# Performance work log

Hardware: AMD Instinct MI355X
Metric: run time of the kernel (lower is better)

The kernel has to match this reference:

```python
import jax, jax.numpy as jnp
import numpy as np

D_STATE = 128   # Mamba2 default (the SS2D d_state=16 is never forwarded to Mamba2)
N_HEADS = 4     # d_ssm // headdim = d_model / (d_model//4)
D_CONV = 4
EPS = 1e-5


def silu(v):
    return v * jax.nn.sigmoid(v)


def setup_inputs() -> dict:
    key = jax.random.key(0)
    ks = jax.random.split(key, 12)
    d_model = 256
    d_inner = 2 * d_model            # expand=2
    d_ssm = d_model
    conv_dim = d_ssm + 2 * D_STATE   # 512
    d_in_proj = 2 * d_inner + 2 * D_STATE + N_HEADS  # 1284
    B, H, W = 8, 64, 64
    inp = {
        "x": jax.random.normal(ks[0], (B, d_model, H, W), jnp.float32),
        "in_proj_w": jax.random.normal(ks[1], (d_in_proj, d_model), jnp.float32) * 0.02,
        "conv_w": jax.random.normal(ks[2], (conv_dim, D_CONV), jnp.float32) * 0.2,
        "conv_b": jnp.zeros((conv_dim,), jnp.float32),
        "dt_bias": jax.random.normal(ks[3], (N_HEADS,), jnp.float32) * 0.1,
        "A_log": jnp.log(jax.random.uniform(ks[4], (N_HEADS,), jnp.float32, 1.0, 16.0)),
        "D": jax.random.normal(ks[5], (N_HEADS,), jnp.float32),
        "norm_w": jnp.ones((d_ssm,), jnp.float32),
        "out_proj_w": jax.random.normal(ks[6], (d_model, d_inner), jnp.float32) * 0.02,
        "se_w1": jax.random.normal(ks[7], (d_model // 4, d_model), jnp.float32) * 0.05,
        "se_b1": jnp.zeros((d_model // 4,), jnp.float32),
        "se_w2": jax.random.normal(ks[8], (d_model, d_model // 4), jnp.float32) * 0.05,
        "se_b2": jnp.zeros((d_model,), jnp.float32),
    }
    return inp


def _forward(x, in_proj_w, conv_w, conv_b, dt_bias, A_log, D, norm_w,
             out_proj_w, se_w1, se_b1, se_w2, se_b2):
    Bb, C, H, W = x.shape
    L = H * W
    d_model = C
    d_inner = 2 * d_model
    d_ssm = d_model
    d_mlp = d_inner - d_ssm
    headdim = d_ssm // N_HEADS
    conv_dim = d_ssm + 2 * D_STATE

    u = x.reshape(Bb, C, L).transpose(0, 2, 1)              # (b, l, c)
    zxbcdt = u @ in_proj_w.T                                 # (b, l, 1284)
    z0 = zxbcdt[..., :d_mlp]
    x0 = zxbcdt[..., d_mlp:2 * d_mlp]
    z = zxbcdt[..., 2 * d_mlp:2 * d_mlp + d_ssm]
    xBC = zxbcdt[..., 2 * d_mlp + d_ssm:2 * d_mlp + d_ssm + conv_dim]
    dt = zxbcdt[..., -N_HEADS:]

    dt = jax.nn.softplus(dt + dt_bias)                       # (b, l, h)

    # causal depthwise conv along l, kernel size D_CONV
    xpad = jnp.pad(xBC, ((0, 0), (D_CONV - 1, 0), (0, 0)))
    xconv = conv_b
    for k in range(D_CONV):
        xconv = xconv + xpad[:, k:k + L, :] * conv_w[:, k]
    xconv = silu(xconv)

    xs = xconv[..., :d_ssm]
    Bm = xconv[..., d_ssm:d_ssm + D_STATE]                   # (b, l, n) ngroups=1
    Cm = xconv[..., d_ssm + D_STATE:]                        # (b, l, n)
    xh = xs.reshape(Bb, L, N_HEADS, headdim)                 # (b, l, h, p)

    A = -jnp.exp(A_log)                                      # (h,)

    def step(hstate, inp):
        xt, dtt, Bt, Ct = inp  # (b,h,p), (b,h), (b,n), (b,n)
        dA = jnp.exp(dtt * A)                                # (b, h)
        hstate = hstate * dA[:, :, None, None] + \
            (dtt[:, :, None, None] * xt[..., None]) * Bt[:, None, None, :]
        y = jnp.einsum('bhpn,bn->bhp', hstate, Ct)
        return hstate, y

    h0 = jnp.zeros((Bb, N_HEADS, headdim, D_STATE), x.dtype)
    _, ys = jax.lax.scan(
        step, h0,
        (xh.transpose(1, 0, 2, 3), dt.transpose(1, 0, 2),
         Bm.transpose(1, 0, 2), Cm.transpose(1, 0, 2)))
    y = ys.transpose(1, 0, 2, 3)                             # (b, l, h, p)
    y = y + D[None, None, :, None] * xh                      # skip
    y = y.reshape(Bb, L, d_ssm)

    # gated RMSNorm (norm_before_gate=False): gate then normalize
    y = y * silu(z)
    y = y * jax.lax.rsqrt(jnp.mean(y * y, axis=-1, keepdims=True) + EPS) * norm_w

    y = jnp.concatenate([silu(z0) * x0, y], axis=-1)         # (b, l, d_inner)
    out = y @ out_proj_w.T                                   # (b, l, d_model)
    out = out.transpose(0, 2, 1).reshape(Bb, C, H, W)

    # SE-style spectral attention
    s = out.mean(axis=(2, 3))                                # (b, c)
    s = jax.nn.relu(s @ se_w1.T + se_b1)
    s = jax.nn.sigmoid(s @ se_w2.T + se_b2)
    return out * s[:, :, None, None]


def reference(x, in_proj_w, conv_w, conv_b, dt_bias, A_log, D, norm_w,
              out_proj_w, se_w1, se_b1, se_w2, se_b2):
    return _forward(x, in_proj_w, conv_w, conv_b, dt_bias, A_log, D, norm_w,
                    out_proj_w, se_w1, se_b1, se_w2, se_b2)
```

## Files before the change

### kernel.cpp

```cpp
#include <hip/hip_runtime.h>
#include <stdint.h>

typedef __attribute__((ext_vector_type(8))) short bf16x8;
typedef __attribute__((ext_vector_type(4))) float f32x4;

__device__ __forceinline__ float bf2f(unsigned short u) {
  unsigned int x = ((unsigned int)u) << 16;
  return __builtin_bit_cast(float, x);
}
__device__ __forceinline__ unsigned short f2bf(float f) {
  unsigned int x = __builtin_bit_cast(unsigned int, f);
  unsigned int r = x + 0x7FFFu + ((x >> 16) & 1u);
  return (unsigned short)(r >> 16);
}
__device__ __forceinline__ float silu(float v) { return v / (1.f + __expf(-v)); }
__device__ __forceinline__ f32x4 fz4() { f32x4 z; z[0]=0.f; z[1]=0.f; z[2]=0.f; z[3]=0.f; return z; }

#define LSEQ 4096
#define DMODEL 256
#define NIN 1284
#define NINP 1408

__global__ __launch_bounds__(256) void k_prep(const float* __restrict__ w_in,
                                              const float* __restrict__ w_out,
                                              unsigned short* __restrict__ wpad,
                                              unsigned short* __restrict__ woutbf,
                                              const float* __restrict__ x,
                                              unsigned short* __restrict__ ubf) {
  int bid = blockIdx.x;
  int tid = threadIdx.x;
  if (bid < 1920) {
    int idx = bid * 256 + tid;
    const int tot1 = NINP * DMODEL;
    if (idx < tot1) {
      int n = idx / DMODEL, k = idx % DMODEL;
      int src = (n < 512) ? ((n & 1) ? 256 + (n >> 1) : (n >> 1)) : n;
      float v = (src < NIN) ? w_in[src * DMODEL + k] : 0.f;
      wpad[idx] = f2bf(v);
    } else {
      int j = idx - tot1;
      woutbf[j] = f2bf(w_out[j]);
    }
    return;
  }
  __shared__ float t[64][65];
  int r = (bid - 1920) & 255;
  int b = (bid - 1920) >> 8;
  int lt = r >> 2, kt = r & 3;
  int l0 = lt * 64, k0 = kt * 64;
  int j = tid & 63, i0 = tid >> 6;
  for (int rr = 0; rr < 16; rr++) {
    int ki = i0 + rr * 4;
    t[ki][j] = x[(size_t)(b * DMODEL + k0 + ki) * LSEQ + l0 + j];
  }
  __syncthreads();
  for (int rr = 0; rr < 16; rr++) {
    int li = i0 + rr * 4;
    ubf[(size_t)(b * LSEQ + l0 + li) * DMODEL + k0 + j] = f2bf(t[j][li]);
  }
}

template <int KDIM, int LDA, int LDB, int EPI>
__global__ __launch_bounds__(256) void k_gemm(const unsigned short* __restrict__ A,
                                              const unsigned short* __restrict__ B,
                                              float* __restrict__ outF,
                                              unsigned short* __restrict__ outBF,
                                              unsigned short* __restrict__ outBF2,
                                              float* __restrict__ dtb, int tilesN) {
  __shared__ __align__(16) short lds[17408];
  short* As = lds;
  short* Bs = lds + 8192;
  int nwg = gridDim.x;
  int orig = blockIdx.x;
  int wgid = (nwg & 7) ? orig : ((orig & 7) * (nwg >> 3) + (orig >> 3));
  int tn = wgid % tilesN, tm = wgid / tilesN;
  int m0 = tm * 128, n0 = tn * 128;
  int tid = threadIdx.x;
  int w = tid >> 6, lane = tid & 63;
  int wr = w >> 1, wc = w & 1;
  f32x4 acc[4][4];
  for (int i = 0; i < 4; i++)
    for (int j = 0; j < 4; j++) acc[i][j] = fz4();

  for (int kt = 0; kt < KDIM / 64; kt++) {
    int k0 = kt * 64;
    for (int i = 0; i < 4; i++) {
      int rowblk = w * 32 + i * 8;
      int row = rowblk + (lane >> 3);
      int kc = ((lane & 7) ^ (row & 7)) * 8;
      const unsigned short* ga = A + (size_t)(m0 + row) * LDA + k0 + kc;
      __builtin_amdgcn_global_load_lds((const __attribute__((address_space(1))) unsigned int*)ga,
                                       (__attribute__((address_space(3))) unsigned int*)&As[rowblk * 64],
                                       16, 0, 0);
      const unsigned short* gb = B + (size_t)(n0 + row) * LDB + k0 + kc;
      __builtin_amdgcn_global_load_lds((const __attribute__((address_space(1))) unsigned int*)gb,
                                       (__attribute__((address_space(3))) unsigned int*)&Bs[rowblk * 64],
                                       16, 0, 0);
    }
    __syncthreads();
    for (int kk = 0; kk < 64; kk += 32) {
      int gq = (kk >> 3) + (lane >> 4);
      bf16x8 af[4], bfr[4];
      for (int mi = 0; mi < 4; mi++) {
        int rt = wr * 64 + mi * 16 + (lane & 15);
        af[mi] = *(const bf16x8*)((const char*)As + rt * 128 + ((gq ^ (rt & 7)) << 4));
      }
      for (int ni = 0; ni < 4; ni++) {
        int rs = wc * 64 + ni * 16 + (lane & 15);
        bfr[ni] = *(const bf16x8*)((const char*)Bs + rs * 128 + ((gq ^ (rs & 7)) << 4));
      }
      for (int mi = 0; mi < 4; mi++)
        for (int ni = 0; ni < 4; ni++)
          acc[mi][ni] = __builtin_amdgcn_mfma_f32_16x16x32_bf16(af[mi], bfr[ni], acc[mi][ni], 0, 0, 0);
    }
    __syncthreads();
  }

  int fq = lane >> 4, fr = lane & 15;
  if constexpr (EPI == 1) {
    short* Ct = lds;
    for (int mi = 0; mi < 4; mi++)
      for (int ni = 0; ni < 4; ni++)
        for (int j = 0; j < 4; j++) {
          int r = wr * 64 + mi * 16 + fq * 4 + j;
          int cch = wc * 64 + ni * 16 + fr;
          Ct[cch * 136 + r] = (short)f2bf(acc[mi][ni][j]);
        }
    __syncthreads();
    int b = m0 >> 12, l0 = m0 & 4095;
    for (int it = 0; it < 4; it++) {
      int row = it * 32 + (tid >> 3);
      int cc = (tid & 7) * 16;
      uint4 v0 = *(const uint4*)&Ct[row * 136 + cc];
      uint4 v1 = *(const uint4*)&Ct[row * 136 + cc + 8];
      unsigned short* dst = outBF + ((size_t)(b * 256 + n0 + row)) * 4096 + l0 + cc;
      *(uint4*)dst = v0;
      *(uint4*)&dst[8] = v1;
    }
  } else if constexpr (EPI == 2) {
    unsigned short* xbc = (unsigned short*)outF;
    if (n0 >= 1280) {
      if (wc == 0 && fr < 4) {
        for (int mi = 0; mi < 4; mi++)
          for (int j = 0; j < 4; j++) {
            int m = m0 + wr * 64 + mi * 16 + fq * 4 + j;
            dtb[m * 4 + fr] = acc[mi][0][j];
          }
      }
    } else if (n0 < 512) {
      short* Ct = lds;
      for (int mi = 0; mi < 4; mi++)
        for (int ni = 0; ni < 4; ni++)
          for (int j = 0; j < 4; j++) {
            float v = acc[mi][ni][j];
            float vp = __shfl_xor(v, 1, 64);
            if (!(fr & 1)) {
              float zc = silu(v) * vp;
              Ct[(wr * 64 + mi * 16 + fq * 4 + j) * 72 + wc * 32 + ni * 8 + (fr >> 1)] =
                  (short)f2bf(zc);
            }
          }
      __syncthreads();
      int r = tid >> 1, base = (tid & 1) * 32;
      for (int it = 0; it < 4; it++) {
        int cc = base + it * 8;
        uint4 v = *(const uint4*)&Ct[r * 72 + cc];
        *(uint4*)&outBF[(size_t)(m0 + r) * 512 + (n0 >> 1) + cc] = v;
      }
    } else {
      short* Ct = lds;
      for (int mi = 0; mi < 4; mi++)
        for (int ni = 0; ni < 4; ni++)
          for (int j = 0; j < 4; j++)
            Ct[(wr * 64 + mi * 16 + fq * 4 + j) * 136 + wc * 64 + ni * 16 + fr] =
                (short)f2bf(acc[mi][ni][j]);
      __syncthreads();
      int rr = tid >> 4, cc = (tid & 15) * 8;
      for (int it = 0; it < 8; it++) {
        int r = it * 16 + rr;
        uint4 v = *(const uint4*)&Ct[r * 136 + cc];
        if (n0 < 768) *(uint4*)&outBF2[(size_t)(m0 + r) * 256 + (n0 - 512) + cc] = v;
        else *(uint4*)&xbc[(size_t)(m0 + r) * 512 + (n0 - 768) + cc] = v;
      }
    }
  } else {
    bool dttile = (n0 >= 1280);
    if (dttile) {
      if (wc == 0 && fr < 4) {
        for (int mi = 0; mi < 4; mi++)
          for (int j = 0; j < 4; j++) {
            int m = m0 + wr * 64 + mi * 16 + fq * 4 + j;
            dtb[m * 4 + fr] = acc[mi][0][j];
          }
      }
    } else {
      short* Ct = lds;
      for (int mi = 0; mi < 4; mi++)
        for (int ni = 0; ni < 4; ni++)
          for (int j = 0; j < 4; j++)
            Ct[(wr * 64 + mi * 16 + fq * 4 + j) * 136 + wc * 64 + ni * 16 + fr] =
                (short)f2bf(acc[mi][ni][j]);
      __syncthreads();
      int rr = tid >> 4, cc = (tid & 15) * 8;
      for (int it = 0; it < 8; it++) {
        int r = it * 16 + rr;
        uint4 v = *(const uint4*)&Ct[r * 136 + cc];
        *(uint4*)&outBF[(size_t)(m0 + r) * 1280 + n0 + cc] = v;
      }
    }
  }
}

__global__ __launch_bounds__(256) void k_conv(const unsigned short* __restrict__ src, int stride,
                                              const float* __restrict__ conv_w,
                                              const float* __restrict__ conv_b,
                                              unsigned short* __restrict__ xs,
                                              unsigned short* __restrict__ bc,
                                              unsigned short* __restrict__ xsT,
                                              unsigned short* __restrict__ bT,
                                              const float* __restrict__ dtraw,
                                              const float* __restrict__ dt_bias,
                                              const float* __restrict__ A_log,
                                              float* __restrict__ dts,
                                              float* __restrict__ cums) {
  __shared__ __align__(16) unsigned short xt[35 * 512];
  int bid = blockIdx.x;
  int tid = threadIdx.x;
  if (bid >= 1024) {
    int w4 = tid >> 6, lane = tid & 63;
    int gc = (bid - 1024) * 4 + w4;
    int bh = gc >> 6, cc = gc & 63;
    int b2 = bh >> 2, h2 = bh & 3;
    int t = cc * 64 + lane;
    float v = dtraw[(size_t)(b2 * LSEQ + t) * 4 + h2] + dt_bias[h2];
    float dt = (v > 20.f) ? v : log1pf(__expf(v));
    float Ah = -__expf(A_log[h2]);
    float s = dt * Ah;
    for (int off = 1; off < 64; off <<= 1) {
      float o = __shfl_up(s, off, 64);
      if (lane >= off) s += o;
    }
    dts[bh * LSEQ + t] = dt;
    cums[bh * LSEQ + t] = s;
    return;
  }
  int b = bid >> 7;
  int t0 = (bid & 127) * 32;
  for (int id = tid; id < 35 * 64; id += 256) {
    int r = id >> 6, ch = id & 63;
    int t = t0 - 3 + r;
    float4 v;
    if (t < 0) v = make_float4(0.f, 0.f, 0.f, 0.f);
    else v = *(const float4*)&src[(size_t)(b * LSEQ + t) * stride + ch * 8];
    *(float4*)&xt[r * 512 + ch * 8] = v;
  }
  __syncthreads();
  int c0 = tid, c1 = tid + 256;
  float w0[4], w1[4];
  for (int k = 0; k < 4; k++) { w0[k] = conv_w[c0 * 4 + k]; w1[k] = conv_w[c1 * 4 + k]; }
  float bb0 = conv_b[c0], bb1 = conv_b[c1];
  unsigned short xa0[32], xa1[32];
#pragma unroll
  for (int tl = 0; tl < 32; tl++) {
    float a0 = bb0, a1 = bb1;
    for (int k = 0; k < 4; k++) {
      a0 += bf2f(xt[(tl + k) * 512 + c0]) * w0[k];
      a1 += bf2f(xt[(tl + k) * 512 + c1]) * w1[k];
    }
    a0 = silu(a0); a1 = silu(a1);
    unsigned short u0 = f2bf(a0), u1 = f2bf(a1);
    xa0[tl] = u0; xa1[tl] = u1;
    size_t row = (size_t)(b * LSEQ + t0 + tl);
    xs[row * 256 + c0] = u0;
    bc[row * 256 + (c1 - 256)] = u1;
  }
  if (xsT) {
    const uint4* p0 = (const uint4*)xa0;
    for (int k = 0; k < 4; k++)
      *(uint4*)&xsT[((size_t)(b * 256 + c0)) * LSEQ + t0 + k * 8] = p0[k];
    if (c1 < 384) {
      const uint4* p1 = (const uint4*)xa1;
      for (int k = 0; k < 4; k++)
        *(uint4*)&bT[((size_t)(b * 128 + (c1 - 256))) * LSEQ + t0 + k * 8] = p1[k];
    }
  }
}

__global__ __launch_bounds__(256) void k_scan(const unsigned short* __restrict__ xs,
                                              const unsigned short* __restrict__ bc,
// ... 137 lines not shown
    bf16x8 xf[4];
#pragma unroll
    for (int ni = 0; ni < 4; ni++) {
      int rp = ni * 16 + (lane & 15);
      xf[ni] = *(const bf16x8*)((char*)XT + rp * 128 + ((g ^ (rp & 7)) << 4));
    }
    {
      bf16x8 a = *(const bf16x8*)((char*)Ms + rt * 128 + ((g ^ (rt & 7)) << 4));
#pragma unroll
      for (int ni = 0; ni < 4; ni++)
        acc2[ni] = __builtin_amdgcn_mfma_f32_16x16x32_bf16(a, xf[ni], acc2[ni], 0, 0, 0);
    }
    {
      bf16x8 a3 = xf[w];
#pragma unroll
      for (int ni = 0; ni < 8; ni++) {
        int rn = ni * 16 + (lane & 15);
        bf16x8 bfr = *(const bf16x8*)((char*)BTs + rn * 128 + ((g ^ (rn & 7)) << 4));
        acc3[ni] = __builtin_amdgcn_mfma_f32_16x16x32_bf16(a3, bfr, acc3[ni], 0, 0, 0);
      }
    }
  }
  __syncthreads();
  unsigned short* STst = sh;
#pragma unroll
  for (int ni = 0; ni < 4; ni++)
#pragma unroll
    for (int j = 0; j < 4; j++) {
      int t = w * 16 + (lane >> 4) * 4 + j;
      int p = ni * 16 + (lane & 15);
      Ms[t * 72 + p] = f2bf(acc2[ni][j]);
    }
#pragma unroll
  for (int ni = 0; ni < 8; ni++)
#pragma unroll
    for (int j = 0; j < 4; j++) {
      int p = w * 16 + (lane >> 4) * 4 + j;
      int n = ni * 16 + (lane & 15);
      STst[p * 136 + n] = f2bf(acc3[ni][j]);
    }
  __syncthreads();
  {
    int rr = tid >> 3, cc = (tid & 7) * 8;
    for (int it = 0; it < 2; it++) {
      int t = it * 32 + rr;
      uint4 v = *(const uint4*)&Ms[t * 72 + cc];
      *(uint4*)&yb[(size_t)(m0 + t) * 256 + h * 64 + cc] = v;
    }
  }
  {
    unsigned short* stp = ST + ((size_t)bid << 13);
    int rr = tid >> 2, cc = (tid & 3) * 32;
    for (int q = 0; q < 4; q++) {
      uint4 v = *(const uint4*)&STst[rr * 136 + cc + q * 8];
      *(uint4*)&stp[rr * 128 + cc + q * 8] = v;
    }
  }
}

__global__ __launch_bounds__(256) void k_chunkB(const unsigned short* __restrict__ ST,
                                                const float* __restrict__ cums,
                                                unsigned short* __restrict__ HT) {
  int bid = blockIdx.x;
  int bh = bid >> 3, psl = bid & 7;
  int p = psl * 8 + (threadIdx.x >> 5);
  int n0 = (threadIdx.x & 31) * 4;
  float H[4] = {0.f, 0.f, 0.f, 0.f};
  for (int c = 0; c < 64; c++) {
    size_t base = (size_t)(bh * 64 + c);
    ushort4 hv;
    unsigned short* ha = (unsigned short*)&hv;
#pragma unroll
    for (int e = 0; e < 4; e++) ha[e] = f2bf(H[e]);
    *(ushort4*)&HT[(base * 64 + p) * 128 + n0] = hv;
    ushort4 s4 = *(const ushort4*)&ST[(base << 13) + p * 128 + n0];
    float dec = __expf(cums[bh * LSEQ + c * 64 + 63]);
    H[0] = H[0] * dec + bf2f(s4.x);
    H[1] = H[1] * dec + bf2f(s4.y);
    H[2] = H[2] * dec + bf2f(s4.z);
    H[3] = H[3] * dec + bf2f(s4.w);
  }
}

__global__ __launch_bounds__(256) void k_chunkC(const unsigned short* __restrict__ bc,
                                                const unsigned short* __restrict__ xs,
                                                const unsigned short* __restrict__ HT,
                                                const float* __restrict__ cums,
                                                const float* __restrict__ Dp,
                                                unsigned short* __restrict__ yb) {
  __shared__ __align__(16) unsigned short Hs[64 * 128];
  __shared__ __align__(16) unsigned short yst[64 * 72];
  int bid = blockIdx.x;
  int bh = bid >> 6, c = bid & 63;
  int b = bh >> 2, h = bh & 3;
  int m0 = b * LSEQ + c * 64;
  int tid = threadIdx.x, w = tid >> 6, lane = tid & 63;
  float Dh = Dp[h];
  for (int it = 0; it < 4; it++) {
    int idx = it * 256 + tid, row = idx >> 4, g = idx & 15;
    uint4 v = *(const uint4*)&HT[((size_t)(bh * 64 + c) * 64 + row) * 128 + g * 8];
    *(uint4*)((char*)Hs + row * 256 + ((g ^ (row & 7)) << 4)) = v;
  }
  float exq[4];
  {
    int tb = w * 16 + (lane >> 4) * 4;
#pragma unroll
    for (int j = 0; j < 4; j++) exq[j] = __expf(cums[bh * LSEQ + c * 64 + tb + j]);
  }
  __syncthreads();
  int rt = w * 16 + (lane & 15);
  const unsigned short* arow = bc + (size_t)(m0 + rt) * 256 + 128;
  f32x4 acc[4];
#pragma unroll
  for (int i = 0; i < 4; i++) acc[i] = fz4();
#pragma unroll
  for (int ks = 0; ks < 4; ks++) {
    int g = ks * 4 + (lane >> 4);
    bf16x8 a = *(const bf16x8*)&arow[g * 8];
#pragma unroll
    for (int ni = 0; ni < 4; ni++) {
      int rp = ni * 16 + (lane & 15);
      bf16x8 bfr = *(const bf16x8*)((char*)Hs + rp * 256 + ((g ^ (rp & 7)) << 4));
      acc[ni] = __builtin_amdgcn_mfma_f32_16x16x32_bf16(a, bfr, acc[ni], 0, 0, 0);
    }
  }
#pragma unroll
  for (int ni = 0; ni < 4; ni++)
#pragma unroll
    for (int j = 0; j < 4; j++) {
      int t = w * 16 + (lane >> 4) * 4 + j;
      int p = ni * 16 + (lane & 15);
      yst[t * 72 + p] = f2bf(acc[ni][j] * exq[j]);
    }
  __syncthreads();
  {
    int rr = tid >> 3, cc = (tid & 7) * 8;
    for (int it = 0; it < 2; it++) {
      int t = it * 32 + rr;
      size_t off = (size_t)(m0 + t) * 256 + h * 64 + cc;
      uint4 yo = *(const uint4*)&yb[off];
      uint4 xv = *(const uint4*)&xs[off];
      const unsigned short* pyo = (const unsigned short*)&yo;
      const unsigned short* pxv = (const unsigned short*)&xv;
      const unsigned short* pys = &yst[t * 72 + cc];
      uint4 vo;
      unsigned short* po = (unsigned short*)&vo;
#pragma unroll
      for (int e = 0; e < 8; e++)
        po[e] = f2bf(bf2f(pyo[e]) + bf2f(pys[e]) + Dh * bf2f(pxv[e]));
      *(uint4*)&yb[off] = vo;
    }
  }
}

template <int MODE>
__global__ __launch_bounds__(256) void k_ycat(const unsigned short* __restrict__ y,
                                              const unsigned short* __restrict__ zsrc,
                                              const float* __restrict__ norm_w,
                                              unsigned short* __restrict__ ocat) {
  int bid = blockIdx.x;
  int tid = threadIdx.x, w = tid >> 6, lane = tid & 63;
  size_t m = (size_t)bid * 4 + w;
  int j0 = lane * 4;
  ushort4 yv = *(const ushort4*)&y[m * 256 + j0];
  ushort4 zv;
  if constexpr (MODE == 0) zv = *(const ushort4*)&zsrc[m * 256 + j0];
  else zv = *(const ushort4*)&zsrc[m * 1280 + 512 + j0];
  unsigned short ya[4] = {yv.x, yv.y, yv.z, yv.w};
  unsigned short za[4] = {zv.x, zv.y, zv.z, zv.w};
  float g[4]; float ssum = 0.f;
  for (int i = 0; i < 4; i++) {
    float gg = bf2f(ya[i]) * silu(bf2f(za[i]));
    g[i] = gg; ssum += gg * gg;
  }
  for (int off = 32; off; off >>= 1) ssum += __shfl_xor(ssum, off, 64);
  float inv = rsqrtf(ssum * (1.f / 256.f) + 1e-5f);
  ushort4 o2;
  unsigned short* o2a = (unsigned short*)&o2;
  for (int i = 0; i < 4; i++) o2a[i] = f2bf(g[i] * norm_w[j0 + i] * inv);
  *(ushort4*)&ocat[m * 512 + 256 + j0] = o2;
  if constexpr (MODE == 1) {
    ushort4 p0 = *(const ushort4*)&zsrc[m * 1280 + 2 * j0];
    ushort4 p1 = *(const ushort4*)&zsrc[m * 1280 + 2 * j0 + 4];
    ushort4 o1;
    unsigned short* o1a = (unsigned short*)&o1;
    o1a[0] = f2bf(silu(bf2f(p0.x)) * bf2f(p0.y));
    o1a[1] = f2bf(silu(bf2f(p0.z)) * bf2f(p0.w));
    o1a[2] = f2bf(silu(bf2f(p1.x)) * bf2f(p1.y));
    o1a[3] = f2bf(silu(bf2f(p1.z)) * bf2f(p1.w));
    *(ushort4*)&ocat[m * 512 + j0] = o1;
  }
}

__global__ __launch_bounds__(256) void k_semean(const unsigned short* __restrict__ rest,
                                                float* __restrict__ smean) {
  __shared__ float wsum[4];
  int row = blockIdx.x;
  int tid = threadIdx.x, w = tid >> 6, lane = tid & 63;
  const unsigned short* p = rest + (size_t)row * 4096;
  float acc = 0.f;
  for (int it = 0; it < 2; it++) {
    uint4 v = *(const uint4*)&p[(it * 256 + tid) * 8];
    const unsigned short* pv = (const unsigned short*)&v;
#pragma unroll
    for (int e = 0; e < 8; e++) acc += bf2f(pv[e]);
  }
  for (int off = 32; off; off >>= 1) acc += __shfl_xor(acc, off, 64);
  if (lane == 0) wsum[w] = acc;
  __syncthreads();
  if (tid == 0) smean[row] = wsum[0] + wsum[1] + wsum[2] + wsum[3];
}

__global__ __launch_bounds__(512) void k_sefc(const float* __restrict__ smean,
                                              const float* __restrict__ w1, const float* __restrict__ b1,
                                              const float* __restrict__ w2, const float* __restrict__ b2,
                                              float* __restrict__ s2) {
  __shared__ float s1[512];
  int tid = threadIdx.x;
  int b = tid >> 6, j = tid & 63;
  float acc = b1[j];
  for (int k = 0; k < 256; k++) acc += smean[b * 256 + k] * (1.f / 4096.f) * w1[j * 256 + k];
  s1[b * 64 + j] = fmaxf(acc, 0.f);
  __syncthreads();
  for (int idx = tid; idx < 2048; idx += 512) {
    int bb = idx >> 8, c = idx & 255;
    float a2 = b2[c];
    for (int k = 0; k < 64; k++) a2 += s1[bb * 64 + k] * w2[c * 64 + k];
    s2[idx] = 1.f / (1.f + expf(-a2));
  }
}

__global__ __launch_bounds__(256) void k_final(const unsigned short* __restrict__ rest,
                                               const float* __restrict__ s2,
                                               float* __restrict__ out) {
  int row = blockIdx.x;
  float s = s2[row];
  int tid = threadIdx.x;
  const unsigned short* p = rest + (size_t)row * 4096;
  float* o = out + (size_t)row * 4096;
  for (int it = 0; it < 2; it++) {
    int base = (it * 256 + tid) * 8;
    uint4 v = *(const uint4*)&p[base];
    const unsigned short* pv = (const unsigned short*)&v;
    float4 f0, f1;
    f0.x = bf2f(pv[0]) * s; f0.y = bf2f(pv[1]) * s;
    f0.z = bf2f(pv[2]) * s; f0.w = bf2f(pv[3]) * s;
    f1.x = bf2f(pv[4]) * s; f1.y = bf2f(pv[5]) * s;
    f1.z = bf2f(pv[6]) * s; f1.w = bf2f(pv[7]) * s;
    *(float4*)&o[base] = f0;
    *(float4*)&o[base + 4] = f1;
  }
}

extern "C" void kernel_launch(void* const* d_in, const int* in_sizes, int n_in,
                              void* d_out, int out_size, void* d_ws, size_t ws_size,
                              hipStream_t stream) {
  const float* x         = (const float*)d_in[0];
  const float* in_proj_w = (const float*)d_in[1];
  const float* conv_w    = (const float*)d_in[2];
  const float* conv_b    = (const float*)d_in[3];
  const float* dt_bias   = (const float*)d_in[4];
  const float* A_log     = (const float*)d_in[5];
  const float* Dp        = (const float*)d_in[6];
  const float* norm_w    = (const float*)d_in[7];
  const float* out_projw = (const float*)d_in[8];
  const float* se_w1     = (const float*)d_in[9];
  const float* se_b1     = (const float*)d_in[10];
  const float* se_w2     = (const float*)d_in[11];
  const float* se_b2     = (const float*)d_in[12];
  float* out = (float*)d_out;
  char* ws = (char*)d_ws;

  const size_t NEED_CHUNKED = 220676096;

  if (ws_size >= NEED_CHUNKED) {
    unsigned short* ST16  = (unsigned short*)(ws + 0);
    unsigned short* ubf   = (unsigned short*)(ws + 0);
    unsigned short* xbc   = (unsigned short*)(ws + 16777216);
    unsigned short* res16 = (unsigned short*)(ws + 0);
    unsigned short* zcat  = (unsigned short*)(ws + 67108864);
    unsigned short* zbuf  = (unsigned short*)(ws + 100663296);
    unsigned short* xsb   = (unsigned short*)(ws + 117440512);
    unsigned short* bcb   = (unsigned short*)(ws + 134217728);
    unsigned short* HT    = (unsigned short*)(ws + 150994944);
    unsigned short* xsT   = (unsigned short*)(ws + 150994944);
    unsigned short* bT    = (unsigned short*)(ws + 167772160);
    unsigned short* ybuf  = (unsigned short*)(ws + 184549376);
    unsigned short* wpad  = (unsigned short*)(ws + 201326592);
    unsigned short* woutb = (unsigned short*)(ws + 202047488);
    float*          dtraw = (float*)(ws + 202309632);
    float*          dts   = (float*)(ws + 202833920);
    float*          cums  = (float*)(ws + 203358208);
    float*          smean = (float*)(ws + 203882496);
    float*          s2    = (float*)(ws + 203890688);

    k_prep<<<3968, 256, 0, stream>>>(in_proj_w, out_projw, wpad, woutb, x, ubf);
    k_gemm<256, 256, 256, 2><<<256 * 11, 256, 0, stream>>>(ubf, wpad, (float*)xbc, zcat, zbuf, dtraw, 11);
    k_conv<<<1536, 256, 0, stream>>>(xbc, 512, conv_w, conv_b, xsb, bcb, xsT, bT,
                                     dtraw, dt_bias, A_log, dts, cums);
    k_chunkA<<<2048, 256, 0, stream>>>(bcb, xsT, bT, dts, cums, ST16, ybuf);
    k_chunkB<<<256, 256, 0, stream>>>(ST16, cums, HT);
    k_chunkC<<<2048, 256, 0, stream>>>(bcb, xsb, HT, cums, Dp, ybuf);
    k_ycat<0><<<8192, 256, 0, stream>>>(ybuf, zbuf, norm_w, zcat);
    k_gemm<512, 512, 512, 1><<<256 * 2, 256, 0, stream>>>(zcat, woutb, nullptr, res16, nullptr, nullptr, 2);
    k_semean<<<2048, 256, 0, stream>>>(res16, smean);
    k_sefc<<<1, 512, 0, stream>>>(smean, se_w1, se_b1, se_w2, se_b2, s2);
    k_final<<<2048, 256, 0, stream>>>(res16, s2, out);
  } else {
    unsigned short* ubf   = (unsigned short*)(ws + 0);
    unsigned short* res16 = (unsigned short*)(ws + 0);
    unsigned short* xsb   = (unsigned short*)(ws + 16777216);
    unsigned short* bcb   = (unsigned short*)(ws + 33554432);
    unsigned short* zx    = (unsigned short*)(ws + 50331648);
    float*          dtb   = (float*)(ws + 134217728);
    unsigned short* ybuf  = (unsigned short*)(ws + 134742016);
    unsigned short* ycat  = (unsigned short*)(ws + 151519232);
    unsigned short* wpad  = (unsigned short*)(ws + 185073664);
    unsigned short* woutb = (unsigned short*)(ws + 185794560);
    float*          smean = (float*)(ws + 186056704);
    float*          s2    = (float*)(ws + 186064896);

    k_prep<<<3968, 256, 0, stream>>>(in_proj_w, out_projw, wpad, woutb, x, ubf);
    k_gemm<256, 256, 256, 0><<<256 * 11, 256, 0, stream>>>(ubf, wpad, nullptr, zx, nullptr, dtb, 11);
    k_conv<<<1024, 256, 0, stream>>>(zx + 768, 1280, conv_w, conv_b, xsb, bcb, nullptr, nullptr,
                                     nullptr, nullptr, nullptr, nullptr, nullptr);
    k_scan<<<512, 256, 0, stream>>>(xsb, bcb, dtb, dt_bias, A_log, Dp, ybuf);
    k_ycat<1><<<8192, 256, 0, stream>>>(ybuf, zx, norm_w, ycat);
    k_gemm<512, 512, 512, 1><<<256 * 2, 256, 0, stream>>>(ycat, woutb, nullptr, res16, nullptr, nullptr, 2);
    k_semean<<<2048, 256, 0, stream>>>(res16, smean);
    k_sefc<<<1, 512, 0, stream>>>(smean, se_w1, se_b1, se_w2, se_b2, s2);
    k_final<<<2048, 256, 0, stream>>>(res16, s2, out);
  }
}
```

Before: 221.0 us.

## Replace in_proj GEMM with persistent row-block kernel reusing A across all N tiles

Replaces the 2816-workgroup in_proj GEMM with a 256-workgroup, 512-thread kernel. Each workgroup loads its 128x256 A row block into LDS and registers once, then sweeps all 11 N tiles. B tiles are double-buffered through direct global-to-LDS loads. The aim is to stop re-reading A for every N tile and to overlap B loads with MFMA. The trade-offs are only 256 workgroups, high register pressure from holding all of A, a serialized per-tile epilogue with extra barriers, and xbc moved to a new workspace offset.

```diff
diff --git a/kernel.cpp b/kernel.cpp
--- a/kernel.cpp
+++ b/kernel.cpp
@@ -57,6 +57,170 @@
   for (int rr = 0; rr < 16; rr++) {
     int li = i0 + rr * 4;
     ubf[(size_t)(b * LSEQ + l0 + li) * DMODEL + k0 + j] = f2bf(t[j][li]);
+  }
+}
+
+__global__ __launch_bounds__(512, 2) void k_gemm1p(const unsigned short* __restrict__ A,
+                                                   const unsigned short* __restrict__ Bw,
+                                                   unsigned short* __restrict__ zcat,
+                                                   unsigned short* __restrict__ zbuf,
+                                                   unsigned short* __restrict__ xbc,
+                                                   float* __restrict__ dtb) {
+  __shared__ __align__(16) unsigned short As[32768];
+  __shared__ __align__(16) unsigned short Bb[2][8192];
+  __shared__ __align__(16) unsigned short Ct[8704];
+  int tid = threadIdx.x, w = tid >> 6, lane = tid & 63;
+  int wr = w >> 2, wc = w & 3;
+  int m0 = blockIdx.x * 128;
+
+#pragma unroll
+  for (int i = 0; i < 8; i++) {
+    int r = (w * 8 + i) * 2 + (lane >> 5);
+    int s = lane & 31;
+    int l = (s & ~7) | ((s & 7) ^ (r & 7));
+    const unsigned short* ga = A + (size_t)(m0 + r) * 256 + l * 8;
+    __builtin_amdgcn_global_load_lds((const __attribute__((address_space(1))) unsigned int*)ga,
+                                     (__attribute__((address_space(3))) unsigned int*)&As[(w * 8 + i) * 512],
+                                     16, 0, 0);
+  }
+  auto issueB = [&](int tn, int kt, int buf) {
+#pragma unroll
+    for (int i = 0; i < 2; i++) {
+      int r = (w * 2 + i) * 8 + (lane >> 3);
+      int s = lane & 7;
+      int l = s ^ (r & 7);
+      const unsigned short* gb = Bw + (size_t)(tn * 128 + r) * 256 + kt * 64 + l * 8;
+      __builtin_amdgcn_global_load_lds((const __attribute__((address_space(1))) unsigned int*)gb,
+                                       (__attribute__((address_space(3))) unsigned int*)&Bb[buf][(w * 2 + i) * 512],
+                                       16, 0, 0);
+    }
+  };
+  issueB(0, 0, 0);
+  asm volatile("s_waitcnt vmcnt(2)" ::: "memory");
+  __builtin_amdgcn_s_barrier();
+  asm volatile("" ::: "memory");
+
+  bf16x8 Af[4][2][4];
+#pragma unroll
+  for (int kt = 0; kt < 4; kt++)
+#pragma unroll
+    for (int kk = 0; kk < 2; kk++)
+#pragma unroll
+      for (int mi = 0; mi < 4; mi++) {
+        int rt = wr * 64 + mi * 16 + (lane & 15);
+        int g = kt * 8 + kk * 4 + (lane >> 4);
+        int slot = (g & ~7) | ((g & 7) ^ (rt & 7));
+        Af[kt][kk][mi] = *(const bf16x8*)((const char*)As + rt * 512 + slot * 16);
+      }
+
+  int fq = lane >> 4, fr = lane & 15;
+  f32x4 acc[4][2];
+  for (int tn = 0; tn < 11; tn++) {
+#pragma unroll
+    for (int mi = 0; mi < 4; mi++)
+#pragma unroll
+      for (int ni = 0; ni < 2; ni++) acc[mi][ni] = fz4();
+#pragma unroll
+    for (int kt = 0; kt < 4; kt++) {
+      asm volatile("" ::: "memory");
+      if (!(tn == 10 && kt == 3)) {
+        int ntn = (kt == 3) ? tn + 1 : tn;
+        issueB(ntn, (kt + 1) & 3, (kt + 1) & 1);
+        asm volatile("s_waitcnt vmcnt(2)" ::: "memory");
+      } else {
+        asm volatile("s_waitcnt vmcnt(0)" ::: "memory");
+      }
+      __builtin_amdgcn_s_barrier();
+      asm volatile("" ::: "memory");
+#pragma unroll
+      for (int kk = 0; kk < 2; kk++) {
+#pragma unroll
+        for (int ni = 0; ni < 2; ni++) {
+          int rs = wc * 32 + ni * 16 + (lane & 15);
+          int g2 = kk * 4 + (lane >> 4);
+          int slot2 = g2 ^ (rs & 7);
+          bf16x8 bf = *(const bf16x8*)((const char*)&Bb[kt & 1][0] + rs * 128 + slot2 * 16);
+#pragma unroll
+          for (int mi = 0; mi < 4; mi++)
+            acc[mi][ni] = __builtin_amdgcn_mfma_f32_16x16x32_bf16(Af[kt][kk][mi], bf, acc[mi][ni], 0, 0, 0);
+        }
+      }
+      asm volatile("" ::: "memory");
+      __builtin_amdgcn_s_barrier();
+      asm volatile("" ::: "memory");
+    }
+    int n0 = tn * 128;
+    if (tn == 10) {
+      if (wc == 0 && fr < 4) {
+#pragma unroll
+        for (int mi = 0; mi < 4; mi++)
+#pragma unroll
+          for (int j = 0; j < 4; j++)
+            dtb[(size_t)(m0 + wr * 64 + mi * 16 + fq * 4 + j) * 4 + fr] = acc[mi][0][j];
+      }
+    } else if (tn < 4) {
+      for (int rh = 0; rh < 2; rh++) {
+        if (wr == rh) {
+#pragma unroll
+          for (int mi = 0; mi < 4; mi++)
+#pragma unroll
+            for (int ni = 0; ni < 2; ni++)
+#pragma unroll
+              for (int j = 0; j < 4; j++) {
+                float v = acc[mi][ni][j];
+                float vp = __shfl_xor(v, 1, 64);
+                if (!(lane & 1)) {
+                  float zc = silu(v) * vp;
+                  Ct[(mi * 16 + fq * 4 + j) * 72 + wc * 16 + ni * 8 + (fr >> 1)] = f2bf(zc);
+                }
+              }
+        }
+        asm volatile("s_waitcnt lgkmcnt(0)" ::: "memory");
+        __builtin_amdgcn_s_barrier();
+        asm volatile("" ::: "memory");
+        {
+          int r = tid >> 3, cc = (tid & 7) * 8;
+          uint4 v = *(const uint4*)&Ct[r * 72 + cc];
+          *(uint4*)&zcat[(size_t)(m0 + rh * 64 + r) * 512 + (n0 >> 1) + cc] = v;
+        }
+        asm volatile("" ::: "memory");
+        __builtin_amdgcn_s_barrier();
+        asm volatile("" ::: "memory");
+      }
+    } else {
+      for (int rh = 0; rh < 2; rh++) {
+        if (wr == rh) {
+#pragma unroll
+          for (int mi = 0; mi < 4; mi++)
+#pragma unroll
+            for (int ni = 0; ni < 2; ni++)
+#pragma unroll
+              for (int j = 0; j < 4; j++)
+                Ct[(mi * 16 + fq * 4 + j) * 136 + wc * 32 + ni * 16 + fr] = f2bf(acc[mi][ni][j]);
+        }
+        asm volatile("s_waitcnt lgkmcnt(0)" ::: "memory");
+        __builtin_amdgcn_s_barrier();
+        asm volatile("" ::: "memory");
+        {
+          int r = tid >> 3, cc = (tid & 7) * 16;
+          size_t grow = (size_t)(m0 + rh * 64 + r);
+          uint4 v0 = *(const uint4*)&Ct[r * 136 + cc];
+          uint4 v1 = *(const uint4*)&Ct[r * 136 + cc + 8];
+          if (tn < 6) {
+            unsigned short* d = zbuf + grow * 256 + (n0 - 512) + cc;
+            *(uint4*)d = v0;
+            *(uint4*)(d + 8) = v1;
+          } else {
+            unsigned short* d = xbc + grow * 512 + (n0 - 768) + cc;
+            *(uint4*)d = v0;
+            *(uint4*)(d + 8) = v1;
+          }
+        }
+        asm volatile("" ::: "memory");
+        __builtin_amdgcn_s_barrier();
+        asm volatile("" ::: "memory");
+      }
+    }
   }
 }
 
@@ -118,70 +282,24 @@
 
   int fq = lane >> 4, fr = lane & 15;
   if constexpr (EPI == 1) {
-    short* Ct = lds;
+    short* Ctl = lds;
     for (int mi = 0; mi < 4; mi++)
       for (int ni = 0; ni < 4; ni++)
         for (int j = 0; j < 4; j++) {
           int r = wr * 64 + mi * 16 + fq * 4 + j;
           int cch = wc * 64 + ni * 16 + fr;
-          Ct[cch * 136 + r] = (short)f2bf(acc[mi][ni][j]);
+          Ctl[cch * 136 + r] = (short)f2bf(acc[mi][ni][j]);
         }
     __syncthreads();
     int b = m0 >> 12, l0 = m0 & 4095;
     for (int it = 0; it < 4; it++) {
       int row = it * 32 + (tid >> 3);
       int cc = (tid & 7) * 16;
-      uint4 v0 = *(const uint4*)&Ct[row * 136 + cc];
-      uint4 v1 = *(const uint4*)&Ct[row * 136 + cc + 8];
+      uint4 v0 = *(const uint4*)&Ctl[row * 136 + cc];
+      uint4 v1 = *(const uint4*)&Ctl[row * 136 + cc + 8];
       unsigned short* dst = outBF + ((size_t)(b * 256 + n0 + row)) * 4096 + l0 + cc;
       *(uint4*)dst = v0;
       *(uint4*)&dst[8] = v1;
-    }
-  } else if constexpr (EPI == 2) {
-    unsigned short* xbc = (unsigned short*)outF;
-    if (n0 >= 1280) {
-      if (wc == 0 && fr < 4) {
-        for (int mi = 0; mi < 4; mi++)
-          for (int j = 0; j < 4; j++) {
-            int m = m0 + wr * 64 + mi * 16 + fq * 4 + j;
-            dtb[m * 4 + fr] = acc[mi][0][j];
-          }
-      }
-    } else if (n0 < 512) {
-      short* Ct = lds;
-      for (int mi = 0; mi < 4; mi++)
-        for (int ni = 0; ni < 4; ni++)
-          for (int j = 0; j < 4; j++) {
-            float v = acc[mi][ni][j];
-            float vp = __shfl_xor(v, 1, 64);
-            if (!(fr & 1)) {
-              float zc = silu(v) * vp;
-              Ct[(wr * 64 + mi * 16 + fq * 4 + j) * 72 + wc * 32 + ni * 8 + (fr >> 1)] =
-                  (short)f2bf(zc);
-            }
-          }
-      __syncthreads();
-      int r = tid >> 1, base = (tid & 1) * 32;
-      for (int it = 0; it < 4; it++) {
-        int cc = base + it * 8;
-        uint4 v = *(const uint4*)&Ct[r * 72 + cc];
-        *(uint4*)&outBF[(size_t)(m0 + r) * 512 + (n0 >> 1) + cc] = v;
-      }
-    } else {
-      short* Ct = lds;
-      for (int mi = 0; mi < 4; mi++)
-        for (int ni = 0; ni < 4; ni++)
-          for (int j = 0; j < 4; j++)
-            Ct[(wr * 64 + mi * 16 + fq * 4 + j) * 136 + wc * 64 + ni * 16 + fr] =
-                (short)f2bf(acc[mi][ni][j]);
-      __syncthreads();
-      int rr = tid >> 4, cc = (tid & 15) * 8;
-      for (int it = 0; it < 8; it++) {
-        int r = it * 16 + rr;
-        uint4 v = *(const uint4*)&Ct[r * 136 + cc];
-        if (n0 < 768) *(uint4*)&outBF2[(size_t)(m0 + r) * 256 + (n0 - 512) + cc] = v;
-        else *(uint4*)&xbc[(size_t)(m0 + r) * 512 + (n0 - 768) + cc] = v;
-      }
     }
   } else {
     bool dttile = (n0 >= 1280);
@@ -194,17 +312,17 @@
           }
       }
     } else {
-      short* Ct = lds;
+      short* Ctl = lds;
       for (int mi = 0; mi < 4; mi++)
         for (int ni = 0; ni < 4; ni++)
           for (int j = 0; j < 4; j++)
-            Ct[(wr * 64 + mi * 16 + fq * 4 + j) * 136 + wc * 64 + ni * 16 + fr] =
+            Ctl[(wr * 64 + mi * 16 + fq * 4 + j) * 136 + wc * 64 + ni * 16 + fr] =
                 (short)f2bf(acc[mi][ni][j]);
       __syncthreads();
       int rr = tid >> 4, cc = (tid & 15) * 8;
       for (int it = 0; it < 8; it++) {
         int r = it * 16 + rr;
-        uint4 v = *(const uint4*)&Ct[r * 136 + cc];
+        uint4 v = *(const uint4*)&Ctl[r * 136 + cc];
         *(uint4*)&outBF[(size_t)(m0 + r) * 1280 + n0 + cc] = v;
       }
     }
@@ -702,8 +820,8 @@
   if (ws_size >= NEED_CHUNKED) {
     unsigned short* ST16  = (unsigned short*)(ws + 0);
     unsigned short* ubf   = (unsigned short*)(ws + 0);
-    unsigned short* xbc   = (unsigned short*)(ws + 16777216);
     unsigned short* res16 = (unsigned short*)(ws + 0);
+    unsigned short* xbc   = (unsigned short*)(ws + 33554432);
     unsigned short* zcat  = (unsigned short*)(ws + 67108864);
     unsigned short* zbuf  = (unsigned short*)(ws + 100663296);
     unsigned short* xsb   = (unsigned short*)(ws + 117440512);
@@ -721,7 +839,7 @@
     float*          s2    = (float*)(ws + 203890688);
 
     k_prep<<<3968, 256, 0, stream>>>(in_proj_w, out_projw, wpad, woutb, x, ubf);
-    k_gemm<256, 256, 256, 2><<<256 * 11, 256, 0, stream>>>(ubf, wpad, (float*)xbc, zcat, zbuf, dtraw, 11);
+    k_gemm1p<<<256, 512, 0, stream>>>(ubf, wpad, zcat, zbuf, xbc, dtraw);
     k_conv<<<1536, 256, 0, stream>>>(xbc, 512, conv_w, conv_b, xsb, bcb, xsT, bT,
                                      dtraw, dt_bias, A_log, dts, cums);
     k_chunkA<<<2048, 256, 0, stream>>>(bcb, xsT, bT, dts, cums, ST16, ybuf);
```

New measurement: 241.7 us. +9.3%, slower.

## Fuse chunk output with gated RMSNorm and fold SE mean into out-proj GEMM

Applied to the files above, without the earlier changes.

The chunk-C kernel now processes all four heads per block, so it can apply the D skip, the SiLU(z) gate, the RMSNorm and norm_w directly and write into zcat. This removes the separate k_ycat launch and the round trip of ybuf through memory. The SE channel sum is now computed in the out-proj GEMM epilogue with atomics into smean, which k_prep zeroes, and the k_semean kernel is dropped. The costs are fewer blocks (512 instead of 2048) with sequential per-head work, heavier register use (a 64-float array per thread), and a summation order that depends on atomic timing.

```diff
diff --git a/kernel.cpp b/kernel.cpp
--- a/kernel.cpp
+++ b/kernel.cpp
@@ -26,10 +26,12 @@
                                               unsigned short* __restrict__ wpad,
                                               unsigned short* __restrict__ woutbf,
                                               const float* __restrict__ x,
-                                              unsigned short* __restrict__ ubf) {
+                                              unsigned short* __restrict__ ubf,
+                                              float* __restrict__ smean) {
   int bid = blockIdx.x;
   int tid = threadIdx.x;
   if (bid < 1920) {
+    if (bid < 8) smean[bid * 256 + tid] = 0.f;
     int idx = bid * 256 + tid;
     const int tot1 = NINP * DMODEL;
     if (idx < tot1) {
@@ -118,24 +120,37 @@
 
   int fq = lane >> 4, fr = lane & 15;
   if constexpr (EPI == 1) {
-    short* Ct = lds;
+    short* Ctl = lds;
     for (int mi = 0; mi < 4; mi++)
       for (int ni = 0; ni < 4; ni++)
         for (int j = 0; j < 4; j++) {
           int r = wr * 64 + mi * 16 + fq * 4 + j;
           int cch = wc * 64 + ni * 16 + fr;
-          Ct[cch * 136 + r] = (short)f2bf(acc[mi][ni][j]);
+          Ctl[cch * 136 + r] = (short)f2bf(acc[mi][ni][j]);
         }
     __syncthreads();
     int b = m0 >> 12, l0 = m0 & 4095;
     for (int it = 0; it < 4; it++) {
       int row = it * 32 + (tid >> 3);
       int cc = (tid & 7) * 16;
-      uint4 v0 = *(const uint4*)&Ct[row * 136 + cc];
-      uint4 v1 = *(const uint4*)&Ct[row * 136 + cc + 8];
+      uint4 v0 = *(const uint4*)&Ctl[row * 136 + cc];
+      uint4 v1 = *(const uint4*)&Ctl[row * 136 + cc + 8];
       unsigned short* dst = outBF + ((size_t)(b * 256 + n0 + row)) * 4096 + l0 + cc;
       *(uint4*)dst = v0;
       *(uint4*)&dst[8] = v1;
+    }
+    {
+      int cch = tid >> 1, hf = tid & 1;
+      const short* prow = &Ctl[cch * 136 + hf * 64];
+      float s = 0.f;
+      for (int q = 0; q < 8; q++) {
+        uint4 v = *(const uint4*)&prow[q * 8];
+        const unsigned short* pv = (const unsigned short*)&v;
+#pragma unroll
+        for (int e = 0; e < 8; e++) s += bf2f(pv[e]);
+      }
+      s += __shfl_xor(s, 1, 64);
+      if (!hf) atomicAdd(&dtb[b * 256 + n0 + cch], s);
     }
   } else if constexpr (EPI == 2) {
     unsigned short* xbc = (unsigned short*)outF;
@@ -508,73 +523,105 @@
   }
 }
 
-__global__ __launch_bounds__(256) void k_chunkC(const unsigned short* __restrict__ bc,
-                                                const unsigned short* __restrict__ xs,
-                                                const unsigned short* __restrict__ HT,
-                                                const float* __restrict__ cums,
-                                                const float* __restrict__ Dp,
-                                                unsigned short* __restrict__ yb) {
+__global__ __launch_bounds__(256) void k_chunkC2(const unsigned short* __restrict__ bc,
+                                                 const unsigned short* __restrict__ xs,
+                                                 const unsigned short* __restrict__ zbuf,
+                                                 const unsigned short* __restrict__ HT,
+                                                 const float* __restrict__ cums,
+                                                 const float* __restrict__ Dp,
+                                                 const float* __restrict__ norm_w,
+                                                 const unsigned short* __restrict__ yb,
+                                                 unsigned short* __restrict__ zcat) {
   __shared__ __align__(16) unsigned short Hs[64 * 128];
-  __shared__ __align__(16) unsigned short yst[64 * 72];
+  __shared__ __align__(16) unsigned short yst[64 * 264];
+  __shared__ float nw[256];
   int bid = blockIdx.x;
-  int bh = bid >> 6, c = bid & 63;
-  int b = bh >> 2, h = bh & 3;
+  int b = bid >> 6, c = bid & 63;
   int m0 = b * LSEQ + c * 64;
   int tid = threadIdx.x, w = tid >> 6, lane = tid & 63;
-  float Dh = Dp[h];
-  for (int it = 0; it < 4; it++) {
-    int idx = it * 256 + tid, row = idx >> 4, g = idx & 15;
-    uint4 v = *(const uint4*)&HT[((size_t)(bh * 64 + c) * 64 + row) * 128 + g * 8];
-    *(uint4*)((char*)Hs + row * 256 + ((g ^ (row & 7)) << 4)) = v;
-  }
-  float exq[4];
-  {
-    int tb = w * 16 + (lane >> 4) * 4;
-#pragma unroll
-    for (int j = 0; j < 4; j++) exq[j] = __expf(cums[bh * LSEQ + c * 64 + tb + j]);
-  }
-  __syncthreads();
+  if (tid < 256) nw[tid] = norm_w[tid];
+
   int rt = w * 16 + (lane & 15);
   const unsigned short* arow = bc + (size_t)(m0 + rt) * 256 + 128;
-  f32x4 acc[4];
-#pragma unroll
-  for (int i = 0; i < 4; i++) acc[i] = fz4();
-#pragma unroll
-  for (int ks = 0; ks < 4; ks++) {
-    int g = ks * 4 + (lane >> 4);
-    bf16x8 a = *(const bf16x8*)&arow[g * 8];
-#pragma unroll
-    for (int ni = 0; ni < 4; ni++) {
-      int rp = ni * 16 + (lane & 15);
-      bf16x8 bfr = *(const bf16x8*)((char*)Hs + rp * 256 + ((g ^ (rp & 7)) << 4));
-      acc[ni] = __builtin_amdgcn_mfma_f32_16x16x32_bf16(a, bfr, acc[ni], 0, 0, 0);
-    }
-  }
-#pragma unroll
-  for (int ni = 0; ni < 4; ni++)
-#pragma unroll
-    for (int j = 0; j < 4; j++) {
-      int t = w * 16 + (lane >> 4) * 4 + j;
-      int p = ni * 16 + (lane & 15);
-      yst[t * 72 + p] = f2bf(acc[ni][j] * exq[j]);
-    }
+  bf16x8 af[4];
+#pragma unroll
+  for (int ks = 0; ks < 4; ks++)
+    af[ks] = *(const bf16x8*)&arow[(ks * 4 + (lane >> 4)) * 8];
+
+  for (int h = 0; h < 4; h++) {
+    int bh = b * 4 + h;
+    __syncthreads();
+    for (int it = 0; it < 4; it++) {
+      int idx = it * 256 + tid, row = idx >> 4, g = idx & 15;
+      uint4 v = *(const uint4*)&HT[((size_t)(bh * 64 + c) * 64 + row) * 128 + g * 8];
+      *(uint4*)((char*)Hs + row * 256 + ((g ^ (row & 7)) << 4)) = v;
+    }
+    float exq[4];
+    {
+      int tb = w * 16 + (lane >> 4) * 4;
+#pragma unroll
+      for (int j = 0; j < 4; j++) exq[j] = __expf(cums[bh * LSEQ + c * 64 + tb + j]);
+    }
+    __syncthreads();
+    f32x4 acc[4];
+#pragma unroll
+    for (int i = 0; i < 4; i++) acc[i] = fz4();
+#pragma unroll
+    for (int ks = 0; ks < 4; ks++) {
+      int g = ks * 4 + (lane >> 4);
+#pragma unroll
+      for (int ni = 0; ni < 4; ni++) {
+        int rp = ni * 16 + (lane & 15);
+        bf16x8 bfr = *(const bf16x8*)((char*)Hs + rp * 256 + ((g ^ (rp & 7)) << 4));
+        acc[ni] = __builtin_amdgcn_mfma_f32_16x16x32_bf16(af[ks], bfr, acc[ni], 0, 0, 0);
+      }
+    }
+#pragma unroll
+    for (int ni = 0; ni < 4; ni++)
+#pragma unroll
+      for (int j = 0; j < 4; j++) {
+        int t = w * 16 + (lane >> 4) * 4 + j;
+        int p = ni * 16 + (lane & 15);
+        yst[t * 264 + h * 64 + p] = f2bf(acc[ni][j] * exq[j]);
+      }
+  }
   __syncthreads();
   {
-    int rr = tid >> 3, cc = (tid & 7) * 8;
-    for (int it = 0; it < 2; it++) {
-      int t = it * 32 + rr;
-      size_t off = (size_t)(m0 + t) * 256 + h * 64 + cc;
-      uint4 yo = *(const uint4*)&yb[off];
-      uint4 xv = *(const uint4*)&xs[off];
-      const unsigned short* pyo = (const unsigned short*)&yo;
-      const unsigned short* pxv = (const unsigned short*)&xv;
-      const unsigned short* pys = &yst[t * 72 + cc];
+    int row = tid >> 2, hh = tid & 3;
+    float Dh = Dp[hh];
+    size_t moff = (size_t)(m0 + row) * 256 + hh * 64;
+    const unsigned short* pyst = &yst[row * 264 + hh * 64];
+    float gv[64];
+    float ssum = 0.f;
+#pragma unroll
+    for (int q = 0; q < 8; q++) {
+      uint4 vy = *(const uint4*)&yb[moff + q * 8];
+      uint4 vx = *(const uint4*)&xs[moff + q * 8];
+      uint4 vz = *(const uint4*)&zbuf[moff + q * 8];
+      uint4 vi = *(const uint4*)&pyst[q * 8];
+      const unsigned short* py = (const unsigned short*)&vy;
+      const unsigned short* px = (const unsigned short*)&vx;
+      const unsigned short* pz = (const unsigned short*)&vz;
+      const unsigned short* pi = (const unsigned short*)&vi;
+#pragma unroll
+      for (int e = 0; e < 8; e++) {
+        float yv = bf2f(py[e]) + bf2f(pi[e]) + Dh * bf2f(px[e]);
+        float gg = yv * silu(bf2f(pz[e]));
+        gv[q * 8 + e] = gg;
+        ssum += gg * gg;
+      }
+    }
+    ssum += __shfl_xor(ssum, 1, 64);
+    ssum += __shfl_xor(ssum, 2, 64);
+    float inv = rsqrtf(ssum * (1.f / 256.f) + 1e-5f);
+#pragma unroll
+    for (int q = 0; q < 8; q++) {
       uint4 vo;
       unsigned short* po = (unsigned short*)&vo;
 #pragma unroll
       for (int e = 0; e < 8; e++)
-        po[e] = f2bf(bf2f(pyo[e]) + bf2f(pys[e]) + Dh * bf2f(pxv[e]));
-      *(uint4*)&yb[off] = vo;
+        po[e] = f2bf(gv[q * 8 + e] * nw[hh * 64 + q * 8 + e] * inv);
+      *(uint4*)&zcat[(size_t)(m0 + row) * 512 + 256 + hh * 64 + q * 8] = vo;
     }
   }
 }
@@ -618,25 +665,6 @@
   }
 }
 
-__global__ __launch_bounds__(256) void k_semean(const unsigned short* __restrict__ rest,
-                                                float* __restrict__ smean) {
-  __shared__ float wsum[4];
-  int row = blockIdx.x;
-  int tid = threadIdx.x, w = tid >> 6, lane = tid & 63;
-  const unsigned short* p = rest + (size_t)row * 4096;
-  float acc = 0.f;
-  for (int it = 0; it < 2; it++) {
-    uint4 v = *(const uint4*)&p[(it * 256 + tid) * 8];
-    const unsigned short* pv = (const unsigned short*)&v;
-#pragma unroll
-    for (int e = 0; e < 8; e++) acc += bf2f(pv[e]);
-  }
-  for (int off = 32; off; off >>= 1) acc += __shfl_xor(acc, off, 64);
-  if (lane == 0) wsum[w] = acc;
-  __syncthreads();
-  if (tid == 0) smean[row] = wsum[0] + wsum[1] + wsum[2] + wsum[3];
-}
-
 __global__ __launch_bounds__(512) void k_sefc(const float* __restrict__ smean,
                                               const float* __restrict__ w1, const float* __restrict__ b1,
                                               const float* __restrict__ w2, const float* __restrict__ b2,
@@ -702,8 +730,8 @@
   if (ws_size >= NEED_CHUNKED) {
     unsigned short* ST16  = (unsigned short*)(ws + 0);
     unsigned short* ubf   = (unsigned short*)(ws + 0);
+    unsigned short* res16 = (unsigned short*)(ws + 0);
     unsigned short* xbc   = (unsigned short*)(ws + 16777216);
-    unsigned short* res16 = (unsigned short*)(ws + 0);
     unsigned short* zcat  = (unsigned short*)(ws + 67108864);
     unsigned short* zbuf  = (unsigned short*)(ws + 100663296);
     unsigned short* xsb   = (unsigned short*)(ws + 117440512);
@@ -720,16 +748,14 @@
     float*          smean = (float*)(ws + 203882496);
     float*          s2    = (float*)(ws + 203890688);
 
-    k_prep<<<3968, 256, 0, stream>>>(in_proj_w, out_projw, wpad, woutb, x, ubf);
+    k_prep<<<3968, 256, 0, stream>>>(in_proj_w, out_projw, wpad, woutb, x, ubf, smean);
     k_gemm<256, 256, 256, 2><<<256 * 11, 256, 0, stream>>>(ubf, wpad, (float*)xbc, zcat, zbuf, dtraw, 11);
     k_conv<<<1536, 256, 0, stream>>>(xbc, 512, conv_w, conv_b, xsb, bcb, xsT, bT,
                                      dtraw, dt_bias, A_log, dts, cums);
     k_chunkA<<<2048, 256, 0, stream>>>(bcb, xsT, bT, dts, cums, ST16, ybuf);
     k_chunkB<<<256, 256, 0, stream>>>(ST16, cums, HT);
-    k_chunkC<<<2048, 256, 0, stream>>>(bcb, xsb, HT, cums, Dp, ybuf);
-    k_ycat<0><<<8192, 256, 0, stream>>>(ybuf, zbuf, norm_w, zcat);
-    k_gemm<512, 512, 512, 1><<<256 * 2, 256, 0, stream>>>(zcat, woutb, nullptr, res16, nullptr, nullptr, 2);
-    k_semean<<<2048, 256, 0, stream>>>(res16, smean);
+    k_chunkC2<<<512, 256, 0, stream>>>(bcb, xsb, zbuf, HT, cums, Dp, norm_w, ybuf, zcat);
+    k_gemm<512, 512, 512, 1><<<256 * 2, 256, 0, stream>>>(zcat, woutb, nullptr, res16, nullptr, smean, 2);
     k_sefc<<<1, 512, 0, stream>>>(smean, se_w1, se_b1, se_w2, se_b2, s2);
     k_final<<<2048, 256, 0, stream>>>(res16, s2, out);
   } else {
@@ -746,14 +772,13 @@
     float*          smean = (float*)(ws + 186056704);
     float*          s2    = (float*)(ws + 186064896);
 
-    k_prep<<<3968, 256, 0, stream>>>(in_proj_w, out_projw, wpad, woutb, x, ubf);
+    k_prep<<<3968, 256, 0, stream>>>(in_proj_w, out_projw, wpad, woutb, x, ubf, smean);
     k_gemm<256, 256, 256, 0><<<256 * 11, 256, 0, stream>>>(ubf, wpad, nullptr, zx, nullptr, dtb, 11);
     k_conv<<<1024, 256, 0, stream>>>(zx + 768, 1280, conv_w, conv_b, xsb, bcb, nullptr, nullptr,
                                      nullptr, nullptr, nullptr, nullptr, nullptr);
     k_scan<<<512, 256, 0, stream>>>(xsb, bcb, dtb, dt_bias, A_log, Dp, ybuf);
     k_ycat<1><<<8192, 256, 0, stream>>>(ybuf, zx, norm_w, ycat);
-    k_gemm<512, 512, 512, 1><<<256 * 2, 256, 0, stream>>>(ycat, woutb, nullptr, res16, nullptr, nullptr, 2);
-    k_semean<<<2048, 256, 0, stream>>>(res16, smean);
+    k_gemm<512, 512, 512, 1><<<256 * 2, 256, 0, stream>>>(ycat, woutb, nullptr, res16, nullptr, smean, 2);
     k_sefc<<<1, 512, 0, stream>>>(smean, se_w1, se_b1, se_w2, se_b2, s2);
     k_final<<<2048, 256, 0, stream>>>(res16, s2, out);
   }
```

New measurement: 218.2 us. About the same (-1.3%).
